# Kernel optimization log

Measured on AMD Instinct MI355X. Metric: run time of the kernel, lower is better.

Reference implementation:

```python
import jax, jax.numpy as jnp
import numpy as np

C = 64       # class_number (from json groups)
D = 256      # out_dimension = predicted.shape[1]
N = 262144   # batch size


def setup_inputs() -> dict:
    key = jax.random.key(0)
    k1, k2, k3, k4 = jax.random.split(key, 4)
    predicted = jax.random.normal(k1, (N, D), dtype=jnp.float32)
    target = jax.random.randint(k2, (N,), 0, C)
    centroids = jax.random.normal(k3, (C, D), dtype=jnp.float32)
    # accumulated per-class distance sums are nonnegative (sqrt is applied)
    distances = jax.random.uniform(k4, (C, 1), dtype=jnp.float32) * float(N)
    # count = bincount(target) as the torch module accumulates; clamp >= 1
    ones = jnp.ones((N,), jnp.float32)
    count = jnp.maximum(jax.ops.segment_sum(ones, target, num_segments=C), 1.0)[:, None]
    # build_class_weight_matrix: single group containing every label -> all 1.5
    class_weights = jnp.full((C, C), 1.5, dtype=jnp.float32)
    return dict(predicted=predicted, centroids=centroids, distances=distances,
                count=count, class_weights=class_weights, target=target)


def reference(predicted, centroids, distances, count, class_weights, target):
    # === calculate_loss path (epoch % 3 == 2) ===
    C_ = centroids.shape[0]
    sel_counts = count[target]            # [N,1] gather
    sel_centroids = centroids[target]     # [N,D] gather
    pr = predicted / sel_counts           # [N,D]
    cent_new = centroids.at[target].add(pr)                 # scatter-add
    vec = jnp.linalg.norm(sel_centroids - pr, axis=1)       # [N]
    s = distances.at[target].add(vec[:, None])              # scatter-add [C,1]
    s = jnp.sqrt(s) / count                                 # [C,1]
    # cdist(cent_new, cent_new, p=2) via the norm trick
    sq = jnp.sum(cent_new * cent_new, axis=1)               # [C]
    d2 = jnp.maximum(sq[:, None] + sq[None, :] - 2.0 * (cent_new @ cent_new.T), 0.0)
    mask = ~jnp.eye(C_, dtype=bool)
    m = jnp.sqrt(jnp.where(mask, d2, 1.0))                  # safe off-diagonal sqrt
    S = s + s.T                                             # s[i] + s[j], [C,C]
    term = jnp.where(mask, class_weights * S / m, 0.0)
    sum_ = jnp.sum(term)
    loss = sum_ / C_ * (C_ - 1)
    return loss + jnp.sum(jnp.abs(cent_new)) / 1000000.0
```

## Files before the change

### kernel.cpp

```cpp
#include <hip/hip_runtime.h>
#include <math.h>

#define NROWS 262144
#define DIM   256
#define NC    64
#define CD    (NC*DIM)
#define NBLK  512

#define OFF_CENT   0
#define OFF_SF     16384
#define OFF_ABS    16448
#define OFF_PAIR   16512
#define OFF_SPART  16576
#define OFF_SST2   49344
#define OFF_ST2    50368
#define OFF_PART   115904

typedef short  bf16x8 __attribute__((ext_vector_type(8)));
typedef float  f32x16 __attribute__((ext_vector_type(16)));

#define DPP_ADD(v, ctrl) \
    ((v) + __int_as_float(__builtin_amdgcn_update_dpp(0, __float_as_int(v), (ctrl), 0xf, 0xf, true)))

__device__ __forceinline__ float dpp_sum64(float v) {
    v = DPP_ADD(v, 0x111);
    v = DPP_ADD(v, 0x112);
    v = DPP_ADD(v, 0x114);
    v = DPP_ADD(v, 0x118);
    v = DPP_ADD(v, 0x142);
    v = DPP_ADD(v, 0x143);
    return v;
}

__device__ __forceinline__ unsigned int bf16rne2(float lo, float hi) {
    unsigned int ul = __float_as_uint(lo);
    ul = (ul + 0x7FFFu + ((ul >> 16) & 1u)) >> 16;
    unsigned int uh = __float_as_uint(hi);
    uh = (uh + 0x7FFFu + ((uh >> 16) & 1u)) & 0xFFFF0000u;
    return ul | uh;
}
__device__ __forceinline__ unsigned short bf16rne1(float v) {
    unsigned int x = __float_as_uint(v);
    return (unsigned short)((x + 0x7FFFu + ((x >> 16) & 1u)) >> 16);
}
__device__ __forceinline__ float bflo(unsigned int u) { return __uint_as_float(u << 16); }
__device__ __forceinline__ float bfhi(unsigned int u) { return __uint_as_float(u & 0xFFFF0000u); }
__device__ __forceinline__ float bfup(unsigned short u) { return __uint_as_float(((unsigned int)u) << 16); }

__device__ __forceinline__ void do_mfma_chunk(const unsigned short* pb,
                                              const int* tgts, int rbase,
                                              int lane, int d0,
                                              f32x16& a0r, f32x16& a1r)
{
    const int g8  = (lane >> 5) << 3;
    const int cA  = lane & 31;
    const int cB  = 32 + cA;
    const int col = d0 + cA;
    #pragma unroll
    for (int ks = 0; ks < 4; ++ks) {
        const int rA = rbase + ks * 16 + g8;
        const int t0 = tgts[rA+0], t1 = tgts[rA+1], t2 = tgts[rA+2], t3 = tgts[rA+3];
        const int t4 = tgts[rA+4], t5 = tgts[rA+5], t6 = tgts[rA+6], t7 = tgts[rA+7];
        union { unsigned int u[4]; bf16x8 v; } A0, A1, B;
        A0.u[0] = ((t0==cA)?0x3F80u:0u) | (((t1==cA)?0x3F80u:0u) << 16);
        A0.u[1] = ((t2==cA)?0x3F80u:0u) | (((t3==cA)?0x3F80u:0u) << 16);
        A0.u[2] = ((t4==cA)?0x3F80u:0u) | (((t5==cA)?0x3F80u:0u) << 16);
        A0.u[3] = ((t6==cA)?0x3F80u:0u) | (((t7==cA)?0x3F80u:0u) << 16);
        A1.u[0] = ((t0==cB)?0x3F80u:0u) | (((t1==cB)?0x3F80u:0u) << 16);
        A1.u[1] = ((t2==cB)?0x3F80u:0u) | (((t3==cB)?0x3F80u:0u) << 16);
        A1.u[2] = ((t4==cB)?0x3F80u:0u) | (((t5==cB)?0x3F80u:0u) << 16);
        A1.u[3] = ((t6==cB)?0x3F80u:0u) | (((t7==cB)?0x3F80u:0u) << 16);
        const int kr = ks * 16 + g8;
        #pragma unroll
        for (int p = 0; p < 4; ++p) {
            const unsigned int lo = pb[(kr + 2*p    ) * 256 + col];
            const unsigned int hi = pb[(kr + 2*p + 1) * 256 + col];
            B.u[p] = lo | (hi << 16);
        }
        a0r = __builtin_amdgcn_mfma_f32_32x32x16_bf16(A0.v, B.v, a0r, 0, 0, 0);
        a1r = __builtin_amdgcn_mfma_f32_32x32x16_bf16(A1.v, B.v, a1r, 0, 0, 0);
    }
}

__global__ __launch_bounds__(512, 4)
void k_main(const float* __restrict__ pred, const float* __restrict__ cent,
            const float* __restrict__ count, const int* __restrict__ tgt,
            float* __restrict__ ws)
{
    __shared__ unsigned short pbf[64 * 256];
    __shared__ unsigned short cbf[NC * 256];
    __shared__ int   tgt_s[512];
    __shared__ float inv_s[64];
    __shared__ float vec_s[512];
    __shared__ float sw_s[8][64];

    const int tid  = threadIdx.x;
    const int w    = tid >> 6;
    const int lane = tid & 63;
    const int base = blockIdx.x * 512;

    tgt_s[tid] = tgt[base + tid];
    if (tid < 64) inv_s[tid] = 1.0f / count[tid];
    {
        const float2* c2 = (const float2*)cent;
        unsigned int* cb32 = (unsigned int*)cbf;
        #pragma unroll
        for (int i = 0; i < 16; ++i) {
            const int o = i * 512 + tid;
            const float2 cf = c2[o];
            cb32[o] = bf16rne2(cf.x, cf.y);
        }
    }
    __syncthreads();

    const float4* pred4 = (const float4*)pred;
    const int d0 = w * 32;

    f32x16 acc0 = {};
    f32x16 acc1 = {};

    #pragma unroll 1
    for (int ch = 0; ch < 8; ++ch) {
        const size_t gr = (size_t)(base + ch * 64) * 64 + lane;
        float4 p0 = pred4[gr + (size_t)( 0 + w) * 64];
        float4 p1 = pred4[gr + (size_t)( 8 + w) * 64];
        float4 p2 = pred4[gr + (size_t)(16 + w) * 64];
        float4 p3 = pred4[gr + (size_t)(24 + w) * 64];
        float4 p4 = pred4[gr + (size_t)(32 + w) * 64];
        float4 p5 = pred4[gr + (size_t)(40 + w) * 64];
        float4 p6 = pred4[gr + (size_t)(48 + w) * 64];
        float4 p7 = pred4[gr + (size_t)(56 + w) * 64];

#define ROW(pp, i)                                                             \
        {                                                                      \
            const int rc = 8*(i) + w;                                          \
            const int r  = ch * 64 + rc;                                       \
            const int c  = tgt_s[r];                                           \
            const float iv = inv_s[c];                                         \
            const uint2 cu = *(const uint2*)&cbf[c * 256 + lane * 4];          \
            const float dx = bflo(cu.x) - pp.x * iv;                           \
            const float dy = bfhi(cu.x) - pp.y * iv;                           \
            const float dz = bflo(cu.y) - pp.z * iv;                           \
            const float dw = bfhi(cu.y) - pp.w * iv;                           \
            float ss = dx*dx + dy*dy + dz*dz + dw*dw;                          \
            ss = dpp_sum64(ss);                                                \
            if (lane == 63) vec_s[r] = sqrtf(ss);                              \
            *(uint2*)&pbf[rc * 256 + lane * 4] =                               \
                make_uint2(bf16rne2(pp.x, pp.y), bf16rne2(pp.z, pp.w));        \
        }
        ROW(p0, 0) ROW(p1, 1) ROW(p2, 2) ROW(p3, 3)
        ROW(p4, 4) ROW(p5, 5) ROW(p6, 6) ROW(p7, 7)
#undef ROW
        __syncthreads();
        do_mfma_chunk(pbf, tgt_s, ch * 64, lane, d0, acc0, acc1);
        __syncthreads();
    }

    unsigned short* pp = (unsigned short*)(ws + OFF_PART) + (size_t)blockIdx.x * CD;
    const int dim = d0 + (lane & 31);
    #pragma unroll
    for (int reg = 0; reg < 16; ++reg) {
        const int crow = (reg & 3) + 8 * (reg >> 2) + 4 * (lane >> 5);
        pp[(     crow) * 256 + dim] = bf16rne1(acc0[reg]);
        pp[(32 + crow) * 256 + dim] = bf16rne1(acc1[reg]);
    }

    {
        const float vv = vec_s[w * 64 + lane];
        const int   cc = tgt_s[w * 64 + lane];
        float accs = 0.f;
        for (int k = 0; k < NC; ++k) {
            float sel = (cc == k) ? vv : 0.f;
            sel = dpp_sum64(sel);
            const float tot = __shfl(sel, 63, 64);
            accs += (lane == k) ? tot : 0.f;
        }
        sw_s[w][lane] = accs;
    }
    __syncthreads();
    if (w == 0) {
        float s = 0.f;
        #pragma unroll
        for (int q = 0; q < 8; ++q) s += sw_s[q][lane];
        ws[OFF_SPART + blockIdx.x * 64 + lane] = s;
    }
}

__global__ __launch_bounds__(256)
void k_red(float* __restrict__ ws)
{
    const int b = blockIdx.x, t = threadIdx.x;
    __shared__ float red[4][64];
    if (b < 1024) {
        const int pg = b >> 8, eg = b & 255;
        const int e  = eg * 64 + (t & 63);
        const int ps = t >> 6;
        const unsigned short* pp = (const unsigned short*)(ws + OFF_PART) + e;
        float s = 0.f;
        const int pstart = pg * 128 + ps * 32;
        #pragma unroll 8
        for (int p = pstart; p < pstart + 32; ++p) s += bfup(pp[(size_t)p * CD]);
        red[ps][t & 63] = s;
        __syncthreads();
        if (t < 64)
            ws[OFF_ST2 + pg * CD + eg * 64 + t]
                = red[0][t] + red[1][t] + red[2][t] + red[3][t];
    } else {
        const int q = b - 1024;
        const int c = t & 63, pq = t >> 6;
        float s = 0.f;
        #pragma unroll
        for (int i = 0; i < 8; ++i)
            s += ws[OFF_SPART + (q * 32 + pq * 8 + i) * 64 + c];
        red[pq][c] = s;
        __syncthreads();
        if (t < 64)
            ws[OFF_SST2 + q * 64 + t]
                = red[0][t] + red[1][t] + red[2][t] + red[3][t];
    }
}

__global__ __launch_bounds__(256)
void k2_build(const float* __restrict__ cent, const float* __restrict__ count,
              const float* __restrict__ dist, float* __restrict__ ws)
{
    const int c = blockIdx.x, i = threadIdx.x;
    const float inv = 1.0f / count[c];
    const int o = c * 256 + i;
    float tsum = 0.f;
    #pragma unroll
    for (int pg = 0; pg < 4; ++pg) tsum += ws[OFF_ST2 + pg * CD + o];
    const float val = cent[o] + tsum * inv;
    ws[OFF_CENT + o] = val;
    float a = fabsf(val);
    #pragma unroll
    for (int off = 32; off > 0; off >>= 1) a += __shfl_xor(a, off, 64);
    __shared__ float ra[4];
    if ((i & 63) == 0) ra[i >> 6] = a;
    __syncthreads();
    if (i == 0) {
        float sv = 0.f;
        #pragma unroll
        for (int q = 0; q < 16; ++q) sv += ws[OFF_SST2 + q * 64 + c];
        ws[OFF_ABS + c] = ra[0] + ra[1] + ra[2] + ra[3];
        ws[OFF_SF  + c] = sqrtf(dist[c] + sv) / count[c];
    }
}

__global__ __launch_bounds__(256)
void k3_pairs(const float* __restrict__ cw, float* __restrict__ ws)
{
    const int i    = blockIdx.x;
    const int tid  = threadIdx.x;
    const int lane = tid & 63;
    const int w    = tid >> 6;
    const float4* c4 = (const float4*)(ws + OFF_CENT);
    const float*  sf = ws + OFF_SF;

    float4 ci = c4[i * 64 + lane];
    float  si = sf[i];
    float acc = 0.f;
    for (int j = w; j < NC; j += 4) {
        if (j == i) continue;
        float4 cj = c4[j * 64 + lane];
        float dx = ci.x - cj.x, dy = ci.y - cj.y;
        float dz = ci.z - cj.z, dw = ci.w - cj.w;
        float ss = dx*dx + dy*dy + dz*dz + dw*dw;
        #pragma unroll
        for (int o = 32; o > 0; o >>= 1) ss += __shfl_xor(ss, o, 64);
        acc += cw[i * NC + j] * (si + sf[j]) / sqrtf(ss);
    }
    __shared__ float wsum[4];
    if (lane == 0) wsum[w] = acc;
    __syncthreads();
    if (tid == 0) ws[OFF_PAIR + i] = wsum[0] + wsum[1] + wsum[2] + wsum[3];
}

__global__ __launch_bounds__(64)
void k4_final(const float* __restrict__ ws, float* __restrict__ out)
{
    const int t = threadIdx.x;
    float a = ws[OFF_ABS + t];
    float p = ws[OFF_PAIR + t];
    #pragma unroll
    for (int o = 32; o > 0; o >>= 1) {
        a += __shfl_xor(a, o, 64);
        p += __shfl_xor(p, o, 64);
    }
    if (t == 0) out[0] = p / 64.0f * 63.0f + a * 1e-6f;
}

extern "C" void kernel_launch(void* const* d_in, const int* in_sizes, int n_in,
                              void* d_out, int out_size, void* d_ws, size_t ws_size,
                              hipStream_t stream)
{
    const float* pred  = (const float*)d_in[0];
    const float* cent  = (const float*)d_in[1];
    const float* dist  = (const float*)d_in[2];
    const float* count = (const float*)d_in[3];
    const float* cw    = (const float*)d_in[4];
    const int*   tgt   = (const int*)d_in[5];
    float* ws  = (float*)d_ws;
    float* out = (float*)d_out;

    k_main  <<<NBLK, 512, 0, stream>>>(pred, cent, count, tgt, ws);
    k_red   <<<1040, 256, 0, stream>>>(ws);
    k2_build<<<NC,   256, 0, stream>>>(cent, count, dist, ws);
    k3_pairs<<<NC,   256, 0, stream>>>(cw, ws);
    k4_final<<<1,     64, 0, stream>>>(ws, out);
}
```

Measured before the change: 78.35 us.

## Fuse partial reduction and centroid build into one kernel, drop intermediate stage

Merges the two-stage partial reduction (k_red into ST2/SST2 buffers) and the k2_build kernel into a single kernel with 257 blocks. Each block reduces all 512 bf16 partials for 64 elements and directly writes the updated centroid values and per-64-element abs sums. One extra block computes the per-class scale factors. This removes one launch and the intermediate global round trip. In exchange each block runs a 128-deep serial reduction per thread with less parallelism (257 blocks instead of 1040), and the final kernel now sums 256 abs partials.

```diff
diff --git a/kernel.cpp b/kernel.cpp
--- a/kernel.cpp
+++ b/kernel.cpp
@@ -10,11 +10,9 @@
 #define OFF_CENT   0
 #define OFF_SF     16384
 #define OFF_ABS    16448
-#define OFF_PAIR   16512
-#define OFF_SPART  16576
-#define OFF_SST2   49344
-#define OFF_ST2    50368
-#define OFF_PART   115904
+#define OFF_PAIR   16704
+#define OFF_SPART  16768
+#define OFF_PART   49536
 
 typedef short  bf16x8 __attribute__((ext_vector_type(8)));
 typedef float  f32x16 __attribute__((ext_vector_type(16)));
@@ -187,63 +185,44 @@
 }
 
 __global__ __launch_bounds__(256)
-void k_red(float* __restrict__ ws)
+void k_redbuild(const float* __restrict__ cent, const float* __restrict__ count,
+                const float* __restrict__ dist, float* __restrict__ ws)
 {
     const int b = blockIdx.x, t = threadIdx.x;
     __shared__ float red[4][64];
-    if (b < 1024) {
-        const int pg = b >> 8, eg = b & 255;
-        const int e  = eg * 64 + (t & 63);
+    if (b < 256) {
+        const int e  = b * 64 + (t & 63);
         const int ps = t >> 6;
         const unsigned short* pp = (const unsigned short*)(ws + OFF_PART) + e;
         float s = 0.f;
-        const int pstart = pg * 128 + ps * 32;
+        const int pstart = ps * 128;
         #pragma unroll 8
-        for (int p = pstart; p < pstart + 32; ++p) s += bfup(pp[(size_t)p * CD]);
+        for (int p = pstart; p < pstart + 128; ++p) s += bfup(pp[(size_t)p * CD]);
         red[ps][t & 63] = s;
         __syncthreads();
-        if (t < 64)
-            ws[OFF_ST2 + pg * CD + eg * 64 + t]
-                = red[0][t] + red[1][t] + red[2][t] + red[3][t];
+        if (t < 64) {
+            const float tot = red[0][t] + red[1][t] + red[2][t] + red[3][t];
+            const int o = b * 64 + t;
+            const int c = o >> 8;
+            const float inv = 1.0f / count[c];
+            const float val = cent[o] + tot * inv;
+            ws[OFF_CENT + o] = val;
+            float a = fabsf(val);
+            a = dpp_sum64(a);
+            if (t == 63) ws[OFF_ABS + b] = a;
+        }
     } else {
-        const int q = b - 1024;
-        const int c = t & 63, pq = t >> 6;
+        const int c = t & 63, g = t >> 6;
         float s = 0.f;
-        #pragma unroll
-        for (int i = 0; i < 8; ++i)
-            s += ws[OFF_SPART + (q * 32 + pq * 8 + i) * 64 + c];
-        red[pq][c] = s;
-        __syncthreads();
-        if (t < 64)
-            ws[OFF_SST2 + q * 64 + t]
-                = red[0][t] + red[1][t] + red[2][t] + red[3][t];
-    }
-}
-
-__global__ __launch_bounds__(256)
-void k2_build(const float* __restrict__ cent, const float* __restrict__ count,
-              const float* __restrict__ dist, float* __restrict__ ws)
-{
-    const int c = blockIdx.x, i = threadIdx.x;
-    const float inv = 1.0f / count[c];
-    const int o = c * 256 + i;
-    float tsum = 0.f;
-    #pragma unroll
-    for (int pg = 0; pg < 4; ++pg) tsum += ws[OFF_ST2 + pg * CD + o];
-    const float val = cent[o] + tsum * inv;
-    ws[OFF_CENT + o] = val;
-    float a = fabsf(val);
-    #pragma unroll
-    for (int off = 32; off > 0; off >>= 1) a += __shfl_xor(a, off, 64);
-    __shared__ float ra[4];
-    if ((i & 63) == 0) ra[i >> 6] = a;
-    __syncthreads();
-    if (i == 0) {
-        float sv = 0.f;
-        #pragma unroll
-        for (int q = 0; q < 16; ++q) sv += ws[OFF_SST2 + q * 64 + c];
-        ws[OFF_ABS + c] = ra[0] + ra[1] + ra[2] + ra[3];
-        ws[OFF_SF  + c] = sqrtf(dist[c] + sv) / count[c];
+        const int pstart = g * 128;
+        #pragma unroll 8
+        for (int p = pstart; p < pstart + 128; ++p) s += ws[OFF_SPART + p * 64 + c];
+        red[g][c] = s;
+        __syncthreads();
+        if (t < 64) {
+            const float sv = red[0][t] + red[1][t] + red[2][t] + red[3][t];
+            ws[OFF_SF + t] = sqrtf(dist[t] + sv) / count[t];
+        }
     }
 }
 
@@ -276,18 +255,25 @@
     if (tid == 0) ws[OFF_PAIR + i] = wsum[0] + wsum[1] + wsum[2] + wsum[3];
 }
 
-__global__ __launch_bounds__(64)
+__global__ __launch_bounds__(256)
 void k4_final(const float* __restrict__ ws, float* __restrict__ out)
 {
     const int t = threadIdx.x;
     float a = ws[OFF_ABS + t];
-    float p = ws[OFF_PAIR + t];
+    float p = (t < 64) ? ws[OFF_PAIR + t] : 0.f;
     #pragma unroll
     for (int o = 32; o > 0; o >>= 1) {
         a += __shfl_xor(a, o, 64);
         p += __shfl_xor(p, o, 64);
     }
-    if (t == 0) out[0] = p / 64.0f * 63.0f + a * 1e-6f;
+    __shared__ float ra[4], rp[4];
+    if ((t & 63) == 0) { ra[t >> 6] = a; rp[t >> 6] = p; }
+    __syncthreads();
+    if (t == 0) {
+        float ps = rp[0] + rp[1] + rp[2] + rp[3];
+        float as = ra[0] + ra[1] + ra[2] + ra[3];
+        out[0] = ps / 64.0f * 63.0f + as * 1e-6f;
+    }
 }
 
 extern "C" void kernel_launch(void* const* d_in, const int* in_sizes, int n_in,
@@ -303,9 +289,8 @@
     float* ws  = (float*)d_ws;
     float* out = (float*)d_out;
 
-    k_main  <<<NBLK, 512, 0, stream>>>(pred, cent, count, tgt, ws);
-    k_red   <<<1040, 256, 0, stream>>>(ws);
-    k2_build<<<NC,   256, 0, stream>>>(cent, count, dist, ws);
-    k3_pairs<<<NC,   256, 0, stream>>>(cw, ws);
-    k4_final<<<1,     64, 0, stream>>>(ws, out);
-}
+    k_main    <<<NBLK, 512, 0, stream>>>(pred, cent, count, tgt, ws);
+    k_redbuild<<<257,  256, 0, stream>>>(cent, count, dist, ws);
+    k3_pairs  <<<NC,   256, 0, stream>>>(cw, ws);
+    k4_final  <<<1,    256, 0, stream>>>(ws, out);
+}
```

New measurement: 82.97 us. 5.9% more time.
